# Kernel tuning notes

Measured on AMD Instinct MI355X. Metric: run time of the kernel, lower is better.

The kernel has to match this reference:

```python
import jax, jax.numpy as jnp
import numpy as np

N_NODES = 100000
N_EDGES = 1600000
D_IN = 64
D_H = 64
N_CLS = 2


def setup_inputs() -> dict:
    key = jax.random.key(0)
    ks = jax.random.split(key, 12)
    s = 0.05
    return {
        "features": jax.random.normal(ks[0], (N_NODES, D_IN), dtype=jnp.float32),
        "edge_index": jax.random.randint(ks[1], (2, N_EDGES), 0, N_NODES, dtype=jnp.int64),
        # SAGE layer 1: Linear(2*D_IN, D_H)
        "W1": jax.random.normal(ks[2], (D_H, 2 * D_IN), dtype=jnp.float32) * s,
        "b1": jnp.zeros((D_H,), dtype=jnp.float32),
        # SAGE layer 2: Linear(2*D_H, D_H)
        "W2": jax.random.normal(ks[3], (D_H, 2 * D_H), dtype=jnp.float32) * s,
        "b2": jnp.zeros((D_H,), dtype=jnp.float32),
        # classifier: Linear(D_H, D_H//2) -> ReLU -> Linear(D_H//2, N_CLS)
        "Wc1": jax.random.normal(ks[4], (D_H // 2, D_H), dtype=jnp.float32) * s,
        "bc1": jnp.zeros((D_H // 2,), dtype=jnp.float32),
        "Wc2": jax.random.normal(ks[5], (N_CLS, D_H // 2), dtype=jnp.float32) * s,
        "bc2": jnp.zeros((N_CLS,), dtype=jnp.float32),
    }


def _sage_layer(x, edge_index, W, b):
    # gather src features, scatter-mean into dst, concat with self, linear
    src, dst = edge_index[0], edge_index[1]
    n = x.shape[0]
    ones = jnp.ones(src.shape[0], dtype=x.dtype)
    deg = jax.ops.segment_sum(ones, dst, num_segments=n)
    deg = jnp.maximum(deg, 1.0)  # clamp(min=1)
    neigh = jax.ops.segment_sum(x[src], dst, num_segments=n) / deg[:, None]
    combined = jnp.concatenate([x, neigh], axis=-1)  # [n, 2*d]
    return combined @ W.T + b


def reference(features, edge_index, W1, b1, W2, b2, Wc1, bc1, Wc2, bc2):
    # two SAGE layers with ReLU (dropout = identity at eval)
    x = jax.nn.relu(_sage_layer(features, edge_index, W1, b1))
    x = jax.nn.relu(_sage_layer(x, edge_index, W2, b2))
    # classifier head (embedding_projection unused when return_embeddings=False)
    h = jax.nn.relu(x @ Wc1.T + bc1)
    logits = h @ Wc2.T + bc2
    return logits
```

## Files before the change

### kernel.cpp

```cpp
#include <hip/hip_runtime.h>

#define D 64

__device__ __forceinline__ float bcast(float v, int l) {
    return __uint_as_float(__builtin_amdgcn_readlane(__float_as_uint(v), l));
}

__global__ void __launch_bounds__(256) scatter_kernel(
    const float* __restrict__ x,
    const int*   __restrict__ src,
    const int*   __restrict__ dst,
    float*       __restrict__ agg,
    float*       __restrict__ deg,
    int nedges)
{
    int lane = threadIdx.x & 63;
    int wid  = (blockIdx.x * blockDim.x + threadIdx.x) >> 6;
    int nw   = (gridDim.x * blockDim.x) >> 6;
    for (int e = wid; e < nedges; e += nw) {
        int s = src[e];
        int d = dst[e];
        float v = x[(size_t)s * D + lane];
        atomicAdd(&agg[(size_t)d * D + lane], v);
        if (deg != nullptr && lane == 0) atomicAdd(&deg[d], 1.0f);
    }
}

template <bool RELU>
__global__ void __launch_bounds__(256) lin_kernel(
    const float* __restrict__ x,
    const float* __restrict__ agg,
    const float* __restrict__ deg,
    const float* __restrict__ W,
    const float* __restrict__ b,
    float*       __restrict__ out,
    int n)
{
    __shared__ float4 Wt4[32 * 64];
    __shared__ float  bs[64];
    float* Wt = (float*)Wt4;
    for (int i = threadIdx.x; i < 64 * 128; i += blockDim.x) {
        int j = i >> 7, k = i & 127;
        Wt[(k >> 2) * 256 + j * 4 + (k & 3)] = W[i];
    }
    if (threadIdx.x < 64) bs[threadIdx.x] = b[threadIdx.x];
    __syncthreads();

    int lane = threadIdx.x & 63;
    int wid  = (blockIdx.x * blockDim.x + threadIdx.x) >> 6;
    int nw   = (gridDim.x * blockDim.x) >> 6;
    for (int node = wid; node < n; node += nw) {
        float xv = x[(size_t)node * D + lane];
        float dg = fmaxf(deg[node], 1.0f);
        float av = agg[(size_t)node * D + lane] / dg;
        float sum = bs[lane];
        #pragma unroll
        for (int k4 = 0; k4 < 16; ++k4) {
            float4 w = Wt4[k4 * 64 + lane];
            sum = fmaf(bcast(xv, 4 * k4 + 0), w.x, sum);
            sum = fmaf(bcast(xv, 4 * k4 + 1), w.y, sum);
            sum = fmaf(bcast(xv, 4 * k4 + 2), w.z, sum);
            sum = fmaf(bcast(xv, 4 * k4 + 3), w.w, sum);
        }
        #pragma unroll
        for (int k4 = 16; k4 < 32; ++k4) {
            float4 w = Wt4[k4 * 64 + lane];
            int kk = 4 * (k4 - 16);
            sum = fmaf(bcast(av, kk + 0), w.x, sum);
            sum = fmaf(bcast(av, kk + 1), w.y, sum);
            sum = fmaf(bcast(av, kk + 2), w.z, sum);
            sum = fmaf(bcast(av, kk + 3), w.w, sum);
        }
        out[(size_t)node * D + lane] = RELU ? fmaxf(sum, 0.0f) : sum;
    }
}

__global__ void __launch_bounds__(256) head_kernel(
    const float* __restrict__ x2,
    const float* __restrict__ Wc1,
    const float* __restrict__ bc1,
    const float* __restrict__ Wc2,
    const float* __restrict__ bc2,
    float*       __restrict__ out,
    int n)
{
    __shared__ float w1[32 * 64];
    __shared__ float b1s[32];
    __shared__ float w2[64];
    __shared__ float b2s[2];
    for (int i = threadIdx.x; i < 32 * 64; i += blockDim.x) w1[i] = Wc1[i];
    if (threadIdx.x < 32) b1s[threadIdx.x] = bc1[threadIdx.x];
    if (threadIdx.x < 64) w2[threadIdx.x] = Wc2[threadIdx.x];
    if (threadIdx.x < 2)  b2s[threadIdx.x] = bc2[threadIdx.x];
    __syncthreads();

    int t0     = blockIdx.x * blockDim.x + threadIdx.x;
    int stride = gridDim.x * blockDim.x;
    for (int node = t0; node < n; node += stride) {
        float xr[64];
        const float4* xp = (const float4*)(x2 + (size_t)node * D);
        #pragma unroll
        for (int q = 0; q < 16; ++q) {
            float4 v = xp[q];
            xr[4*q+0] = v.x; xr[4*q+1] = v.y; xr[4*q+2] = v.z; xr[4*q+3] = v.w;
        }
        float l0 = b2s[0], l1 = b2s[1];
        for (int j = 0; j < 32; ++j) {
            float h = b1s[j];
            #pragma unroll
            for (int k = 0; k < 64; ++k) h = fmaf(xr[k], w1[j * 64 + k], h);
            h = fmaxf(h, 0.0f);
            l0 = fmaf(h, w2[j], l0);
            l1 = fmaf(h, w2[32 + j], l1);
        }
        out[(size_t)node * 2 + 0] = l0;
        out[(size_t)node * 2 + 1] = l1;
    }
}

extern "C" void kernel_launch(void* const* d_in, const int* in_sizes, int n_in,
                              void* d_out, int out_size, void* d_ws, size_t ws_size,
                              hipStream_t stream)
{
    const float* feat = (const float*)d_in[0];
    const int*   eidx = (const int*)d_in[1];
    const float* W1   = (const float*)d_in[2];
    const float* b1   = (const float*)d_in[3];
    const float* W2   = (const float*)d_in[4];
    const float* b2   = (const float*)d_in[5];
    const float* Wc1  = (const float*)d_in[6];
    const float* bc1  = (const float*)d_in[7];
    const float* Wc2  = (const float*)d_in[8];
    const float* bc2  = (const float*)d_in[9];

    int n = in_sizes[0] / D;
    int E = in_sizes[1] / 2;
    const int* src = eidx;
    const int* dst = eidx + E;

    float* agg = (float*)d_ws;
    float* x1  = agg + (size_t)n * D;
    float* deg = x1 + (size_t)n * D;

    hipMemsetAsync(agg, 0, (size_t)n * D * sizeof(float), stream);
    hipMemsetAsync(deg, 0, (size_t)n * sizeof(float), stream);
    scatter_kernel<<<2048, 256, 0, stream>>>(feat, src, dst, agg, deg, E);
    lin_kernel<true><<<1024, 256, 0, stream>>>(feat, agg, deg, W1, b1, x1, n);

    hipMemsetAsync(agg, 0, (size_t)n * D * sizeof(float), stream);
    scatter_kernel<<<2048, 256, 0, stream>>>(x1, src, dst, agg, nullptr, E);
    lin_kernel<true><<<1024, 256, 0, stream>>>(x1, agg, deg, W2, b2, agg, n);

    head_kernel<<<391, 256, 0, stream>>>(agg, Wc1, bc1, Wc2, bc2, (float*)d_out, n);
}
```

Baseline: 932.0 us.

## Build CSR by destination and replace atomic scatter with pull-based gather

Builds a CSR adjacency keyed by destination (histogram, two-level scan, fill) once, then each wavefront gathers and averages its neighbors' rows directly, so the per-element float atomics and agg memsets go away. The aggregation is fused with the linear layer, and the classifier head is fused into the second SAGE kernel using lane broadcasts and a shuffle reduction. In exchange it adds several small preprocessing kernels and integer atomics for CSR construction. It also launches 12500 blocks of 512 threads, each reloading the weight matrices into LDS, which adds redundant weight loads and block setup.

Result: slower. 983.5 us (+5.5%).

```diff
diff --git a/kernel.cpp b/kernel.cpp
--- a/kernel.cpp
+++ b/kernel.cpp
@@ -1,58 +1,146 @@
 #include <hip/hip_runtime.h>
 
 #define D 64
+#define TSCAN 1024
+#define NB_SCAN 98
 
 __device__ __forceinline__ float bcast(float v, int l) {
     return __uint_as_float(__builtin_amdgcn_readlane(__float_as_uint(v), l));
 }
 
-__global__ void __launch_bounds__(256) scatter_kernel(
+__global__ void __launch_bounds__(256) hist_kernel(
+    const int* __restrict__ dst, int* __restrict__ cnt, int E)
+{
+    int t = blockIdx.x * blockDim.x + threadIdx.x;
+    int st = gridDim.x * blockDim.x;
+    for (int e = t; e < E; e += st) atomicAdd(&cnt[dst[e]], 1);
+}
+
+__global__ void __launch_bounds__(TSCAN) partial_kernel(
+    const int* __restrict__ cnt, int* __restrict__ partials, int n)
+{
+    __shared__ int red[TSCAN];
+    int i = blockIdx.x * TSCAN + threadIdx.x;
+    red[threadIdx.x] = (i < n) ? cnt[i] : 0;
+    __syncthreads();
+    for (int off = TSCAN / 2; off > 0; off >>= 1) {
+        if (threadIdx.x < off) red[threadIdx.x] += red[threadIdx.x + off];
+        __syncthreads();
+    }
+    if (threadIdx.x == 0) partials[blockIdx.x] = red[0];
+}
+
+__global__ void __launch_bounds__(128) scanp_kernel(
+    const int* __restrict__ partials, int* __restrict__ blockoff, int nb)
+{
+    __shared__ int s[128];
+    int t = threadIdx.x;
+    int orig = (t < nb) ? partials[t] : 0;
+    s[t] = orig;
+    __syncthreads();
+    for (int off = 1; off < 128; off <<= 1) {
+        int v = (t >= off) ? s[t - off] : 0;
+        __syncthreads();
+        s[t] += v;
+        __syncthreads();
+    }
+    if (t < nb) blockoff[t] = s[t] - orig;
+}
+
+__global__ void __launch_bounds__(TSCAN) rowptr_kernel(
+    const int* __restrict__ cnt, const int* __restrict__ blockoff,
+    int* __restrict__ rowptr, int* __restrict__ cursor, int n)
+{
+    __shared__ int s[TSCAN];
+    int b = blockIdx.x;
+    int i = b * TSCAN + threadIdx.x;
+    int v = (i < n) ? cnt[i] : 0;
+    s[threadIdx.x] = v;
+    __syncthreads();
+    for (int off = 1; off < TSCAN; off <<= 1) {
+        int x = (threadIdx.x >= off) ? s[threadIdx.x - off] : 0;
+        __syncthreads();
+        s[threadIdx.x] += x;
+        __syncthreads();
+    }
+    if (i < n) {
+        int excl = blockoff[b] + s[threadIdx.x] - v;
+        rowptr[i] = excl;
+        cursor[i] = excl;
+        if (i == n - 1) rowptr[n] = excl + v;
+    }
+}
+
+__global__ void __launch_bounds__(256) fill_kernel(
+    const int* __restrict__ src, const int* __restrict__ dst,
+    int* __restrict__ cursor, int* __restrict__ adj, int E)
+{
+    int t = blockIdx.x * blockDim.x + threadIdx.x;
+    int st = gridDim.x * blockDim.x;
+    for (int e = t; e < E; e += st) {
+        int p = atomicAdd(&cursor[dst[e]], 1);
+        adj[p] = src[e];
+    }
+}
+
+template <bool HEAD>
+__global__ void __launch_bounds__(512) sage_kernel(
     const float* __restrict__ x,
-    const int*   __restrict__ src,
-    const int*   __restrict__ dst,
-    float*       __restrict__ agg,
-    float*       __restrict__ deg,
-    int nedges)
-{
-    int lane = threadIdx.x & 63;
-    int wid  = (blockIdx.x * blockDim.x + threadIdx.x) >> 6;
-    int nw   = (gridDim.x * blockDim.x) >> 6;
-    for (int e = wid; e < nedges; e += nw) {
-        int s = src[e];
-        int d = dst[e];
-        float v = x[(size_t)s * D + lane];
-        atomicAdd(&agg[(size_t)d * D + lane], v);
-        if (deg != nullptr && lane == 0) atomicAdd(&deg[d], 1.0f);
-    }
-}
-
-template <bool RELU>
-__global__ void __launch_bounds__(256) lin_kernel(
-    const float* __restrict__ x,
-    const float* __restrict__ agg,
-    const float* __restrict__ deg,
+    const int*   __restrict__ rowptr,
+    const int*   __restrict__ adj,
     const float* __restrict__ W,
     const float* __restrict__ b,
+    const float* __restrict__ Wc1,
+    const float* __restrict__ bc1,
+    const float* __restrict__ Wc2,
+    const float* __restrict__ bc2,
     float*       __restrict__ out,
     int n)
 {
-    __shared__ float4 Wt4[32 * 64];
-    __shared__ float  bs[64];
-    float* Wt = (float*)Wt4;
+    extern __shared__ float smem[];
+    float4* Wt4 = (float4*)smem;
+    float*  Wt  = smem;
+    float*  bs  = smem + 8192;
+    float*  wc1t = bs + 64;
+    float*  w2s  = wc1t + 2048;
+    float*  bc1s = w2s + 64;
+    float*  bc2s = bc1s + 32;
+
     for (int i = threadIdx.x; i < 64 * 128; i += blockDim.x) {
         int j = i >> 7, k = i & 127;
         Wt[(k >> 2) * 256 + j * 4 + (k & 3)] = W[i];
     }
     if (threadIdx.x < 64) bs[threadIdx.x] = b[threadIdx.x];
+    if (HEAD) {
+        for (int i = threadIdx.x; i < 32 * 64; i += blockDim.x) {
+            int l = i >> 6, k = i & 63;
+            wc1t[k * 32 + l] = Wc1[i];
+        }
+        if (threadIdx.x < 64) w2s[threadIdx.x] = Wc2[threadIdx.x];
+        if (threadIdx.x < 32) bc1s[threadIdx.x] = bc1[threadIdx.x];
+        if (threadIdx.x < 2)  bc2s[threadIdx.x] = bc2[threadIdx.x];
+    }
     __syncthreads();
 
     int lane = threadIdx.x & 63;
     int wid  = (blockIdx.x * blockDim.x + threadIdx.x) >> 6;
     int nw   = (gridDim.x * blockDim.x) >> 6;
     for (int node = wid; node < n; node += nw) {
+        int ro = rowptr[node], re = rowptr[node + 1];
+        float acc = 0.f;
+        int i = ro;
+        for (; i + 4 <= re; i += 4) {
+            int s0 = adj[i + 0], s1 = adj[i + 1], s2 = adj[i + 2], s3 = adj[i + 3];
+            float v0 = x[(size_t)s0 * D + lane];
+            float v1 = x[(size_t)s1 * D + lane];
+            float v2 = x[(size_t)s2 * D + lane];
+            float v3 = x[(size_t)s3 * D + lane];
+            acc += (v0 + v1) + (v2 + v3);
+        }
+        for (; i < re; ++i) acc += x[(size_t)adj[i] * D + lane];
+        float av = acc / fmaxf((float)(re - ro), 1.0f);
         float xv = x[(size_t)node * D + lane];
-        float dg = fmaxf(deg[node], 1.0f);
-        float av = agg[(size_t)node * D + lane] / dg;
+
         float sum = bs[lane];
         #pragma unroll
         for (int k4 = 0; k4 < 16; ++k4) {
@@ -71,50 +159,29 @@
             sum = fmaf(bcast(av, kk + 2), w.z, sum);
             sum = fmaf(bcast(av, kk + 3), w.w, sum);
         }
-        out[(size_t)node * D + lane] = RELU ? fmaxf(sum, 0.0f) : sum;
-    }
-}
-
-__global__ void __launch_bounds__(256) head_kernel(
-    const float* __restrict__ x2,
-    const float* __restrict__ Wc1,
-    const float* __restrict__ bc1,
-    const float* __restrict__ Wc2,
-    const float* __restrict__ bc2,
-    float*       __restrict__ out,
-    int n)
-{
-    __shared__ float w1[32 * 64];
-    __shared__ float b1s[32];
-    __shared__ float w2[64];
-    __shared__ float b2s[2];
-    for (int i = threadIdx.x; i < 32 * 64; i += blockDim.x) w1[i] = Wc1[i];
-    if (threadIdx.x < 32) b1s[threadIdx.x] = bc1[threadIdx.x];
-    if (threadIdx.x < 64) w2[threadIdx.x] = Wc2[threadIdx.x];
-    if (threadIdx.x < 2)  b2s[threadIdx.x] = bc2[threadIdx.x];
-    __syncthreads();
-
-    int t0     = blockIdx.x * blockDim.x + threadIdx.x;
-    int stride = gridDim.x * blockDim.x;
-    for (int node = t0; node < n; node += stride) {
-        float xr[64];
-        const float4* xp = (const float4*)(x2 + (size_t)node * D);
-        #pragma unroll
-        for (int q = 0; q < 16; ++q) {
-            float4 v = xp[q];
-            xr[4*q+0] = v.x; xr[4*q+1] = v.y; xr[4*q+2] = v.z; xr[4*q+3] = v.w;
-        }
-        float l0 = b2s[0], l1 = b2s[1];
-        for (int j = 0; j < 32; ++j) {
-            float h = b1s[j];
+        float x2 = fmaxf(sum, 0.0f);
+
+        if (!HEAD) {
+            out[(size_t)node * D + lane] = x2;
+        } else {
+            int l = lane & 31;
+            float h = bc1s[l];
             #pragma unroll
-            for (int k = 0; k < 64; ++k) h = fmaf(xr[k], w1[j * 64 + k], h);
+            for (int k = 0; k < 64; ++k)
+                h = fmaf(bcast(x2, k), wc1t[k * 32 + l], h);
             h = fmaxf(h, 0.0f);
-            l0 = fmaf(h, w2[j], l0);
-            l1 = fmaf(h, w2[32 + j], l1);
-        }
-        out[(size_t)node * 2 + 0] = l0;
-        out[(size_t)node * 2 + 1] = l1;
+            float p0 = (lane < 32) ? h * w2s[l]      : 0.0f;
+            float p1 = (lane < 32) ? h * w2s[32 + l] : 0.0f;
+            #pragma unroll
+            for (int off = 1; off < 64; off <<= 1) {
+                p0 += __shfl_xor(p0, off, 64);
+                p1 += __shfl_xor(p1, off, 64);
+            }
+            if (lane == 0) {
+                out[(size_t)node * 2 + 0] = p0 + bc2s[0];
+                out[(size_t)node * 2 + 1] = p1 + bc2s[1];
+            }
+        }
     }
 }
 
@@ -138,18 +205,28 @@
     const int* src = eidx;
     const int* dst = eidx + E;
 
-    float* agg = (float*)d_ws;
-    float* x1  = agg + (size_t)n * D;
-    float* deg = x1 + (size_t)n * D;
-
-    hipMemsetAsync(agg, 0, (size_t)n * D * sizeof(float), stream);
-    hipMemsetAsync(deg, 0, (size_t)n * sizeof(float), stream);
-    scatter_kernel<<<2048, 256, 0, stream>>>(feat, src, dst, agg, deg, E);
-    lin_kernel<true><<<1024, 256, 0, stream>>>(feat, agg, deg, W1, b1, x1, n);
-
-    hipMemsetAsync(agg, 0, (size_t)n * D * sizeof(float), stream);
-    scatter_kernel<<<2048, 256, 0, stream>>>(x1, src, dst, agg, nullptr, E);
-    lin_kernel<true><<<1024, 256, 0, stream>>>(x1, agg, deg, W2, b2, agg, n);
-
-    head_kernel<<<391, 256, 0, stream>>>(agg, Wc1, bc1, Wc2, bc2, (float*)d_out, n);
-}
+    int*   cnt      = (int*)d_ws;
+    int*   partials = cnt + n;
+    int*   blockoff = partials + 128;
+    int*   rowptr   = blockoff + 128;
+    int*   cursor   = rowptr + n + 1;
+    int*   adj      = cursor + n;
+    float* x1       = (float*)(adj + E);
+
+    int nb = (n + TSCAN - 1) / TSCAN;
+
+    hipMemsetAsync(cnt, 0, (size_t)n * sizeof(int), stream);
+    hist_kernel<<<6250, 256, 0, stream>>>(dst, cnt, E);
+    partial_kernel<<<nb, TSCAN, 0, stream>>>(cnt, partials, n);
+    scanp_kernel<<<1, 128, 0, stream>>>(partials, blockoff, nb);
+    rowptr_kernel<<<nb, TSCAN, 0, stream>>>(cnt, blockoff, rowptr, cursor, n);
+    fill_kernel<<<6250, 256, 0, stream>>>(src, dst, cursor, adj, E);
+
+    size_t lds1 = (8192 + 64) * sizeof(float);
+    sage_kernel<false><<<12500, 512, lds1, stream>>>(
+        feat, rowptr, adj, W1, b1, nullptr, nullptr, nullptr, nullptr, x1, n);
+
+    size_t lds2 = (8192 + 64 + 2048 + 64 + 32 + 2) * sizeof(float);
+    sage_kernel<true><<<12500, 512, lds2, stream>>>(
+        x1, rowptr, adj, W2, b2, Wc1, bc1, Wc2, bc2, (float*)d_out, n);
+}
```
